# Kernel tuning notes

Hardware: AMD Instinct MI355X
Metric: run time of the kernel (lower is better)

Reference implementation:

```python
import jax, jax.numpy as jnp
import numpy as np

B, SEQ_LEN, PRED_LEN = 256, 96, 96
ENC_IN, LAG = 8, 1
IN_SIZE = ENC_IN + LAG - 1          # 8
H, L = 512, 2
C_OUT = ENC_IN + LAG                # lstm_c_out = 9
TW = SEQ_LEN + PRED_LEN             # train_window = 192


def _mk(key, shape, scale):
    return (jax.random.normal(key, shape, dtype=jnp.float32) * scale)


def setup_inputs() -> dict:
    key = jax.random.key(0)
    ks = jax.random.split(key, 16)
    s_in = 1.0 / np.sqrt(H)
    bih0 = _mk(ks[5], (4 * H,), s_in).at[H:2 * H].set(1.0)  # forget-gate bias init = 1
    bhh0 = _mk(ks[6], (4 * H,), s_in).at[H:2 * H].set(1.0)
    bih1 = _mk(ks[9], (4 * H,), s_in).at[H:2 * H].set(1.0)
    bhh1 = _mk(ks[10], (4 * H,), s_in).at[H:2 * H].set(1.0)
    return {
        "x_enc": jax.random.normal(ks[0], (B, SEQ_LEN, ENC_IN + LAG), dtype=jnp.float32),
        "x_mark_enc": jax.random.normal(ks[1], (B, SEQ_LEN, 4), dtype=jnp.float32),
        "x_dec": jax.random.normal(ks[2], (B, PRED_LEN, ENC_IN + LAG), dtype=jnp.float32),
        "y_enc": jax.random.normal(ks[3], (B, PRED_LEN, ENC_IN + LAG), dtype=jnp.float32),
        "x_mark_dec": jax.random.normal(ks[4], (B, PRED_LEN, 4), dtype=jnp.float32),
        "Wih0": _mk(ks[7], (4 * H, IN_SIZE), s_in),
        "Whh0": _mk(ks[8], (4 * H, H), s_in),
        "bih0": bih0, "bhh0": bhh0,
        "Wih1": _mk(ks[11], (4 * H, H), s_in),
        "Whh1": _mk(ks[12], (4 * H, H), s_in),
        "bih1": bih1, "bhh1": bhh1,
        "Wout": _mk(ks[13], (C_OUT, L * H), 1.0 / np.sqrt(L * H)),
        "bout": _mk(ks[14], (C_OUT,), 1.0 / np.sqrt(L * H)),
    }


def _lstm_cell(x, h, c, Wih, Whh, bih, bhh):
    # gates in torch order: i, f, g, o
    g = x @ Wih.T + bih + h @ Whh.T + bhh           # [B, 4H]
    i, f, gg, o = jnp.split(g, 4, axis=-1)
    c_new = jax.nn.sigmoid(f) * c + jax.nn.sigmoid(i) * jnp.tanh(gg)
    h_new = jax.nn.sigmoid(o) * jnp.tanh(c_new)
    return h_new, c_new


def reference(x_enc, x_mark_enc, x_dec, y_enc, x_mark_dec,
              Wih0, Whh0, bih0, bhh0, Wih1, Whh1, bih1, bhh1, Wout, bout):
    # get_input_data
    batch = jnp.concatenate([x_enc, y_enc[:, -PRED_LEN:, :]], axis=1)  # [B, TW, enc_in+lag]
    train_batch = batch[:, :, :-1]                                     # [B, TW, IN_SIZE]
    xs = jnp.transpose(train_batch, (1, 0, 2))                         # [TW, B, IN_SIZE]

    h0 = jnp.zeros((B, H), jnp.float32)
    init = (h0, h0, h0, h0)  # (h_l0, c_l0, h_l1, c_l1)

    def step(carry, x_t):
        hl0, cl0, hl1, cl1 = carry
        hl0, cl0 = _lstm_cell(x_t, hl0, cl0, Wih0, Whh0, bih0, bhh0)
        hl1, cl1 = _lstm_cell(hl0, hl1, cl1, Wih1, Whh1, bih1, bhh1)
        hidden = jnp.stack([hl0, hl1], axis=0)                 # [L, B, H]
        # get_hidden_permute: permute(1,2,0).view(B, H*L)
        hp = jnp.transpose(hidden, (1, 2, 0)).reshape(B, H * L)
        return (hl0, cl0, hl1, cl1), hp

    _, hps = jax.lax.scan(step, init, xs)                      # [TW, B, H*L]
    hps = jnp.transpose(hps, (1, 0, 2))                        # [B, TW, H*L]
    output_steps = hps @ Wout.T + bout                         # [B, TW, C_OUT]
    return output_steps, batch  # (output_steps, labels_batch); stop_flag always False
```

## Files before the change

kernel.cpp:

```cpp
#include <hip/hip_runtime.h>
#include <hip/hip_cooperative_groups.h>
#include <cstdint>

namespace cg = cooperative_groups;


typedef __bf16 bf16x8 __attribute__((ext_vector_type(8)));
typedef float f32x4 __attribute__((ext_vector_type(4)));

#define SLOT 131072

__device__ __forceinline__ uint16_t f2bf(float f) {
    uint32_t u = __builtin_bit_cast(uint32_t, f);
    u += 0x7FFFu + ((u >> 16) & 1u);
    return (uint16_t)(u >> 16);
}
__device__ __forceinline__ float bf2f(uint16_t h) {
    return __builtin_bit_cast(float, (uint32_t)h << 16);
}
__device__ __forceinline__ float sigm(float x) { return 1.0f / (1.0f + expf(-x)); }

__device__ __forceinline__ bf16x8 ld_h16(const uint16_t* p) {
    const uint64_t* q = (const uint64_t*)p;
    uint64_t w0 = __hip_atomic_load(q,     __ATOMIC_RELAXED, __HIP_MEMORY_SCOPE_AGENT);
    uint64_t w1 = __hip_atomic_load(q + 1, __ATOMIC_RELAXED, __HIP_MEMORY_SCOPE_AGENT);
    union { uint64_t u[2]; bf16x8 v; } x;
    x.u[0] = w0; x.u[1] = w1;
    return x.v;
}
__device__ __forceinline__ uint64_t ld_h64(const uint64_t* q) {
    return __hip_atomic_load(q, __ATOMIC_RELAXED, __HIP_MEMORY_SCOPE_AGENT);
}

__global__ void __launch_bounds__(256, 1)
lstm_kernel(const float* __restrict__ x_enc, const float* __restrict__ y_enc,
            const float* __restrict__ Wih0, const float* __restrict__ Whh0,
            const float* __restrict__ bih0, const float* __restrict__ bhh0,
            const float* __restrict__ Wih1, const float* __restrict__ Whh1,
            const float* __restrict__ bih1, const float* __restrict__ bhh1,
            const float* __restrict__ Wout, const float* __restrict__ bout,
            float* __restrict__ out,
            uint32_t* __restrict__ stamp,
            uint16_t* __restrict__ hs0hi, uint16_t* __restrict__ hs0lo,
            uint16_t* __restrict__ hs1hi, uint16_t* __restrict__ hs1lo)
{
    extern __shared__ __align__(16) uint8_t LDS[];
    float* ldsF = (float*)LDS;

    const int tid = threadIdx.x;
    const int bid = blockIdx.x;
    const bool isL0 = (bid < 128);
    const int rb = isL0 ? bid : (bid - 128);
    const int g = rb >> 6;
    const int s = rb & 63;

    const int w  = tid >> 6;
    const int l  = tid & 63;
    const int c  = l & 15;
    const int kg = l >> 4;
    const int h  = c & 7;
    const bool lowc = (c < 8);

    if (isL0) {
        for (int idx = tid; idx < 32 * 512; idx += 256) {
            int j = idx >> 9, k = idx & 511;
            int n = s * 8 + (j & 7) + 512 * (j >> 3);
            float v = Whh0[n * 512 + k];
            uint16_t hi = f2bf(v);
            uint16_t lo = f2bf(v - bf2f(hi));
            uint32_t byte = (uint32_t)(j * 1024 + k * 2) ^ (uint32_t)((j & 7) << 4);
            *(uint16_t*)(LDS + byte) = hi;
            *(uint16_t*)(LDS + 32768 + byte) = lo;
        }
        {
            int j = tid >> 3, k = tid & 7;
            int n = s * 8 + (j & 7) + 512 * (j >> 3);
            ldsF[17408 + tid] = Wih0[n * 8 + k];
        }
    } else {
        for (int idx = tid; idx < 32 * 1024; idx += 256) {
            int j = idx >> 10, k = idx & 1023;
            int n = s * 8 + (j & 7) + 512 * (j >> 3);
            float v = (k < 512) ? Wih1[n * 512 + k] : Whh1[n * 512 + (k - 512)];
            uint16_t hi = f2bf(v);
            uint16_t lo = f2bf(v - bf2f(hi));
            uint32_t byte = (uint32_t)(j * 2048 + k * 2) ^ (uint32_t)((j & 7) << 4);
            *(uint16_t*)(LDS + byte) = hi;
            *(uint16_t*)(LDS + 65536 + byte) = lo;
        }
    }
    float bias[4];
#pragma unroll
    for (int gt = 0; gt < 4; ++gt) {
        int n = s * 8 + h + 512 * gt;
        bias[gt] = isL0 ? (bih0[n] + bhh0[n]) : (bih1[n] + bhh1[n]);
    }
    {
        int idx = bid * 256 + tid;
        __hip_atomic_store(((uint32_t*)(hs0hi + 3 * SLOT)) + idx, 0u, __ATOMIC_RELAXED, __HIP_MEMORY_SCOPE_AGENT);
        __hip_atomic_store(((uint32_t*)(hs0lo + 3 * SLOT)) + idx, 0u, __ATOMIC_RELAXED, __HIP_MEMORY_SCOPE_AGENT);
        __hip_atomic_store(((uint32_t*)(hs1hi + 3 * SLOT)) + idx, 0u, __ATOMIC_RELAXED, __HIP_MEMORY_SCOPE_AGENT);
        __hip_atomic_store(((uint32_t*)(hs1lo + 3 * SLOT)) + idx, 0u, __ATOMIC_RELAXED, __HIP_MEMORY_SCOPE_AGENT);
    }
    if (tid == 0)
        __hip_atomic_store(&stamp[bid * 16], 0u, __ATOMIC_RELAXED, __HIP_MEMORY_SCOPE_AGENT);
    float creg[4] = {0.f, 0.f, 0.f, 0.f};

    cg::grid_group grid = cg::this_grid();
    grid.sync();

    const int j0 = c, j1 = 16 + c;
    const uint32_t sw0 = (uint32_t)((j0 & 7) << 4);
    const uint32_t sw1 = (uint32_t)((j1 & 7) << 4);

    for (int p = 0; p < 194; ++p) {
        if (p > 0) {
            if (tid < 128) {
                int pid = (tid < 64) ? (g * 64 + tid) : (128 + g * 64 + (tid - 64));
                while (__hip_atomic_load(&stamp[pid * 16], __ATOMIC_RELAXED,
                                         __HIP_MEMORY_SCOPE_AGENT) < (uint32_t)p)
                    __builtin_amdgcn_s_sleep(1);
            }
            __syncthreads();
        }

        if (isL0) {
            const int t = p;
            if (t < 192) {
                for (int idx = tid; idx < 1024; idx += 256) {
                    int bl = idx >> 3, ch = idx & 7;
                    int b = g * 128 + bl;
                    ldsF[16384 + idx] = (t < 96)
                        ? x_enc[(b * 96 + t) * 9 + ch]
                        : y_enc[(b * 96 + (t - 96)) * 9 + ch];
                }
                __syncthreads();

                const uint16_t* hbh = hs0hi + ((t + 3) & 3) * SLOT;
                const uint16_t* hbl = hs0lo + ((t + 3) & 3) * SLOT;
                const int ar0 = (g * 128 + w * 32 + c) * 512 + kg * 8;
                const int ar1 = ar0 + 16 * 512;
                const uint32_t bb0 = (uint32_t)(j0 * 1024 + kg * 16);
                const uint32_t bb1 = (uint32_t)(j1 * 1024 + kg * 16);
                f32x4 acc00 = {0.f,0.f,0.f,0.f}, acc01 = acc00, acc10 = acc00, acc11 = acc00;
#pragma unroll
                for (int ks = 0; ks < 16; ++ks) {
                    bf16x8 a0h = ld_h16(hbh + ar0 + ks * 32);
                    bf16x8 a0l = ld_h16(hbl + ar0 + ks * 32);
                    bf16x8 a1h = ld_h16(hbh + ar1 + ks * 32);
                    bf16x8 a1l = ld_h16(hbl + ar1 + ks * 32);
                    uint32_t o0 = (bb0 + ks * 64) ^ sw0;
                    uint32_t o1 = (bb1 + ks * 64) ^ sw1;
                    bf16x8 b0h = *(const bf16x8*)(LDS + o0);
                    bf16x8 b0l = *(const bf16x8*)(LDS + 32768 + o0);
                    bf16x8 b1h = *(const bf16x8*)(LDS + o1);
                    bf16x8 b1l = *(const bf16x8*)(LDS + 32768 + o1);
                    acc00 = __builtin_amdgcn_mfma_f32_16x16x32_bf16(a0h, b0h, acc00, 0, 0, 0);
                    acc00 = __builtin_amdgcn_mfma_f32_16x16x32_bf16(a0h, b0l, acc00, 0, 0, 0);
                    acc00 = __builtin_amdgcn_mfma_f32_16x16x32_bf16(a0l, b0h, acc00, 0, 0, 0);
                    acc00 = __builtin_amdgcn_mfma_f32_16x16x32_bf16(a0l, b0l, acc00, 0, 0, 0);
                    acc01 = __builtin_amdgcn_mfma_f32_16x16x32_bf16(a0h, b1h, acc01, 0, 0, 0);
                    acc01 = __builtin_amdgcn_mfma_f32_16x16x32_bf16(a0h, b1l, acc01, 0, 0, 0);
                    acc01 = __builtin_amdgcn_mfma_f32_16x16x32_bf16(a0l, b1h, acc01, 0, 0, 0);
                    acc01 = __builtin_amdgcn_mfma_f32_16x16x32_bf16(a0l, b1l, acc01, 0, 0, 0);
                    acc10 = __builtin_amdgcn_mfma_f32_16x16x32_bf16(a1h, b0h, acc10, 0, 0, 0);
                    acc10 = __builtin_amdgcn_mfma_f32_16x16x32_bf16(a1h, b0l, acc10, 0, 0, 0);
                    acc10 = __builtin_amdgcn_mfma_f32_16x16x32_bf16(a1l, b0h, acc10, 0, 0, 0);
                    acc10 = __builtin_amdgcn_mfma_f32_16x16x32_bf16(a1l, b0l, acc10, 0, 0, 0);
                    acc11 = __builtin_amdgcn_mfma_f32_16x16x32_bf16(a1h, b1h, acc11, 0, 0, 0);
                    acc11 = __builtin_amdgcn_mfma_f32_16x16x32_bf16(a1h, b1l, acc11, 0, 0, 0);
                    acc11 = __builtin_amdgcn_mfma_f32_16x16x32_bf16(a1l, b1h, acc11, 0, 0, 0);
                    acc11 = __builtin_amdgcn_mfma_f32_16x16x32_bf16(a1l, b1l, acc11, 0, 0, 0);
                }
                float rv0[4], rv1[4];
#pragma unroll
                for (int r = 0; r < 4; ++r) {
                    rv0[r] = __shfl_xor(lowc ? acc10[r] : acc00[r], 8);
                    rv1[r] = __shfl_xor(lowc ? acc11[r] : acc01[r], 8);
                }
                uint32_t* d32h = (uint32_t*)(hs0hi + (t & 3) * SLOT);
                uint32_t* d32l = (uint32_t*)(hs0lo + (t & 3) * SLOT);
#pragma unroll
                for (int r = 0; r < 4; ++r) {
                    float k0 = lowc ? acc00[r] : acc10[r];
                    float k1 = lowc ? acc01[r] : acc11[r];
                    float gi = lowc ? k0 : rv0[r];
                    float gf = lowc ? rv0[r] : k0;
                    float gG = lowc ? k1 : rv1[r];
                    float go = lowc ? rv1[r] : k1;
                    int m  = (lowc ? 0 : 16) + kg * 4 + r;
                    int bl = w * 32 + m;
                    const float* xr = ldsF + 16384 + bl * 8;
                    const float* wi = ldsF + 17408;
                    float xp0 = 0, xp1 = 0, xp2 = 0, xp3 = 0;
#pragma unroll
                    for (int k = 0; k < 8; ++k) {
                        float xv = xr[k];
                        xp0 += xv * wi[(h) * 8 + k];
                        xp1 += xv * wi[(8 + h) * 8 + k];
                        xp2 += xv * wi[(16 + h) * 8 + k];
                        xp3 += xv * wi[(24 + h) * 8 + k];
                    }
                    gi += xp0 + bias[0];
                    gf += xp1 + bias[1];
                    gG += xp2 + bias[2];
                    go += xp3 + bias[3];
                    float cn = sigm(gf) * creg[r] + sigm(gi) * tanhf(gG);
                    float hn = sigm(go) * tanhf(cn);
                    creg[r] = cn;
                    uint16_t hh = f2bf(hn);
                    uint16_t ll = f2bf(hn - bf2f(hh));
                    uint32_t phi = (uint32_t)__shfl_xor((int)(uint32_t)hh, 1);
                    uint32_t plo = (uint32_t)__shfl_xor((int)(uint32_t)ll, 1);
                    int eoff = ((g * 128 + bl) * 512 + s * 8 + (h & ~1)) >> 1;
                    if ((h & 1) == 0)
                        __hip_atomic_store(d32h + eoff, (uint32_t)hh | (phi << 16),
                                           __ATOMIC_RELAXED, __HIP_MEMORY_SCOPE_AGENT);
                    else
                        __hip_atomic_store(d32l + eoff, plo | ((uint32_t)ll << 16),
                                           __ATOMIC_RELAXED, __HIP_MEMORY_SCOPE_AGENT);
                }
            }
            const int t2 = p - 2;
            if (t2 >= 0) {
                float* ps = ldsF + 17664;
                if (tid < 144) {
                    int bi = tid / 72;
                    int rem = tid % 72;
                    int co = rem >> 3, seg = rem & 7;
                    int b = g * 128 + s * 2 + bi;
                    const uint64_t* p0h = (const uint64_t*)(hs0hi + (t2 & 3) * SLOT + b * 512);
                    const uint64_t* p0l = (const uint64_t*)(hs0lo + (t2 & 3) * SLOT + b * 512);
                    const uint64_t* p1h = (const uint64_t*)(hs1hi + (t2 & 3) * SLOT + b * 512);
                    const uint64_t* p1l = (const uint64_t*)(hs1lo + (t2 & 3) * SLOT + b * 512);
                    const float* wr = Wout + co * 1024;
                    float sum = 0.f;
#pragma unroll 4
                    for (int q = seg * 16; q < seg * 16 + 16; ++q) {
                        uint64_t u0 = ld_h64(p0h + q);
                        uint64_t u1 = ld_h64(p0l + q);
                        uint64_t u2 = ld_h64(p1h + q);
                        uint64_t u3 = ld_h64(p1l + q);
#pragma unroll
                        for (int e = 0; e < 4; ++e) {
                            int hh_ = q * 4 + e;
                            float h0v = bf2f((uint16_t)(u0 >> (16 * e))) + bf2f((uint16_t)(u1 >> (16 * e)));
                            float h1v = bf2f((uint16_t)(u2 >> (16 * e))) + bf2f((uint16_t)(u3 >> (16 * e)));
                            sum += h0v * wr[2 * hh_] + h1v * wr[2 * hh_ + 1];
                        }
                    }
                    ps[tid] = sum;
                }
                __syncthreads();
                if (tid < 18) {
                    int bi = tid / 9, co = tid % 9;
                    float tot = bout[co];
#pragma unroll
                    for (int k2 = 0; k2 < 8; ++k2) tot += ps[bi * 72 + co * 8 + k2];
                    out[((g * 128 + s * 2 + bi) * 192 + t2) * 9 + co] = tot;
                }
            }
        } else {
            const int t = p - 1;
            if (t >= 0 && t < 192) {
                const uint16_t* hbah = hs0hi + (t & 3) * SLOT;
                const uint16_t* hbal = hs0lo + (t & 3) * SLOT;
                const uint16_t* hbbh = hs1hi + ((t + 3) & 3) * SLOT;
                const uint16_t* hbbl = hs1lo + ((t + 3) & 3) * SLOT;
                const int ar0 = (g * 128 + w * 32 + c) * 512 + kg * 8;
                const int ar1 = ar0 + 16 * 512;
                const uint32_t bb0 = (uint32_t)(j0 * 2048 + kg * 16);
                const uint32_t bb1 = (uint32_t)(j1 * 2048 + kg * 16);
                f32x4 acc00 = {0.f,0.f,0.f,0.f}, acc01 = acc00, acc10 = acc00, acc11 = acc00;
#pragma unroll
                for (int ks = 0; ks < 32; ++ks) {
                    const uint16_t* hbh = (ks < 16) ? hbah : hbbh;
                    const uint16_t* hbl = (ks < 16) ? hbal : hbbl;
                    int ko = (ks & 15) * 32;
                    bf16x8 a0h = ld_h16(hbh + ar0 + ko);
                    bf16x8 a0l = ld_h16(hbl + ar0 + ko);
                    bf16x8 a1h = ld_h16(hbh + ar1 + ko);
                    bf16x8 a1l = ld_h16(hbl + ar1 + ko);
                    uint32_t o0 = (bb0 + ks * 64) ^ sw0;
                    uint32_t o1 = (bb1 + ks * 64) ^ sw1;
                    bf16x8 b0h = *(const bf16x8*)(LDS + o0);
                    bf16x8 b0l = *(const bf16x8*)(LDS + 65536 + o0);
                    bf16x8 b1h = *(const bf16x8*)(LDS + o1);
                    bf16x8 b1l = *(const bf16x8*)(LDS + 65536 + o1);
                    acc00 = __builtin_amdgcn_mfma_f32_16x16x32_bf16(a0h, b0h, acc00, 0, 0, 0);
                    acc00 = __builtin_amdgcn_mfma_f32_16x16x32_bf16(a0h, b0l, acc00, 0, 0, 0);
                    acc00 = __builtin_amdgcn_mfma_f32_16x16x32_bf16(a0l, b0h, acc00, 0, 0, 0);
                    acc00 = __builtin_amdgcn_mfma_f32_16x16x32_bf16(a0l, b0l, acc00, 0, 0, 0);
                    acc01 = __builtin_amdgcn_mfma_f32_16x16x32_bf16(a0h, b1h, acc01, 0, 0, 0);
                    acc01 = __builtin_amdgcn_mfma_f32_16x16x32_bf16(a0h, b1l, acc01, 0, 0, 0);
                    acc01 = __builtin_amdgcn_mfma_f32_16x16x32_bf16(a0l, b1h, acc01, 0, 0, 0);
                    acc01 = __builtin_amdgcn_mfma_f32_16x16x32_bf16(a0l, b1l, acc01, 0, 0, 0);
                    acc10 = __builtin_amdgcn_mfma_f32_16x16x32_bf16(a1h, b0h, acc10, 0, 0, 0);
                    acc10 = __builtin_amdgcn_mfma_f32_16x16x32_bf16(a1h, b0l, acc10, 0, 0, 0);
                    acc10 = __builtin_amdgcn_mfma_f32_16x16x32_bf16(a1l, b0h, acc10, 0, 0, 0);
                    acc10 = __builtin_amdgcn_mfma_f32_16x16x32_bf16(a1l, b0l, acc10, 0, 0, 0);
                    acc11 = __builtin_amdgcn_mfma_f32_16x16x32_bf16(a1h, b1h, acc11, 0, 0, 0);
                    acc11 = __builtin_amdgcn_mfma_f32_16x16x32_bf16(a1h, b1l, acc11, 0, 0, 0);
                    acc11 = __builtin_amdgcn_mfma_f32_16x16x32_bf16(a1l, b1h, acc11, 0, 0, 0);
                    acc11 = __builtin_amdgcn_mfma_f32_16x16x32_bf16(a1l, b1l, acc11, 0, 0, 0);
                }
                float rv0[4], rv1[4];
#pragma unroll
                for (int r = 0; r < 4; ++r) {
                    rv0[r] = __shfl_xor(lowc ? acc10[r] : acc00[r], 8);
                    rv1[r] = __shfl_xor(lowc ? acc11[r] : acc01[r], 8);
                }
                uint32_t* d32h = (uint32_t*)(hs1hi + (t & 3) * SLOT);
                uint32_t* d32l = (uint32_t*)(hs1lo + (t & 3) * SLOT);
#pragma unroll
                for (int r = 0; r < 4; ++r) {
                    float k0 = lowc ? acc00[r] : acc10[r];
                    float k1 = lowc ? acc01[r] : acc11[r];
                    float gi = (lowc ? k0 : rv0[r]) + bias[0];
                    float gf = (lowc ? rv0[r] : k0) + bias[1];
                    float gG = (lowc ? k1 : rv1[r]) + bias[2];
                    float go = (lowc ? rv1[r] : k1) + bias[3];
                    int m  = (lowc ? 0 : 16) + kg * 4 + r;
                    int bl = w * 32 + m;
                    float cn = sigm(gf) * creg[r] + sigm(gi) * tanhf(gG);
                    float hn = sigm(go) * tanhf(cn);
                    creg[r] = cn;
                    uint16_t hh = f2bf(hn);
                    uint16_t ll = f2bf(hn - bf2f(hh));
                    uint32_t phi = (uint32_t)__shfl_xor((int)(uint32_t)hh, 1);
                    uint32_t plo = (uint32_t)__shfl_xor((int)(uint32_t)ll, 1);
                    int eoff = ((g * 128 + bl) * 512 + s * 8 + (h & ~1)) >> 1;
                    if ((h & 1) == 0)
                        __hip_atomic_store(d32h + eoff, (uint32_t)hh | (phi << 16),
                                           __ATOMIC_RELAXED, __HIP_MEMORY_SCOPE_AGENT);
                    else
                        __hip_atomic_store(d32l + eoff, plo | ((uint32_t)ll << 16),
                                           __ATOMIC_RELAXED, __HIP_MEMORY_SCOPE_AGENT);
                }
            }
        }

        asm volatile("s_waitcnt vmcnt(0)" ::: "memory");
        __syncthreads();
        if (tid == 0)
            __hip_atomic_store(&stamp[bid * 16], (uint32_t)(p + 1),
                               __ATOMIC_RELAXED, __HIP_MEMORY_SCOPE_AGENT);
    }
}

__global__ void __launch_bounds__(256)
copy_batch(const float* __restrict__ x_enc, const float* __restrict__ y_enc,
           float* __restrict__ out)
{
    int idx = blockIdx.x * 256 + threadIdx.x;
    if (idx >= 256 * 192 * 9) return;
    int b = idx / 1728;
    int rem = idx % 1728;
    int t = rem / 9, ch = rem % 9;
    float v = (t < 96) ? x_enc[b * 864 + t * 9 + ch]
                       : y_enc[b * 864 + (t - 96) * 9 + ch];
    out[442368 + idx] = v;
}

extern "C" void kernel_launch(void* const* d_in, const int* in_sizes, int n_in,
                              void* d_out, int out_size, void* d_ws, size_t ws_size,
                              hipStream_t stream) {
    const float* x_enc = (const float*)d_in[0];
    const float* y_enc = (const float*)d_in[3];
    const float* Wih0  = (const float*)d_in[5];
    const float* Whh0  = (const float*)d_in[6];
    const float* bih0  = (const float*)d_in[7];
    const float* bhh0  = (const float*)d_in[8];
    const float* Wih1  = (const float*)d_in[9];
    const float* Whh1  = (const float*)d_in[10];
    const float* bih1  = (const float*)d_in[11];
    const float* bhh1  = (const float*)d_in[12];
    const float* Wout  = (const float*)d_in[13];
    const float* bout  = (const float*)d_in[14];
    float* out = (float*)d_out;
    uint32_t* stamp = (uint32_t*)d_ws;
    uint16_t* hs0hi = (uint16_t*)((uint8_t*)d_ws + 16384);
    uint16_t* hs0lo = hs0hi + 4 * SLOT;
    uint16_t* hs1hi = hs0lo + 4 * SLOT;
    uint16_t* hs1lo = hs1hi + 4 * SLOT;

    hipLaunchKernelGGL(copy_batch, dim3(1728), dim3(256), 0, stream,
                       x_enc, y_enc, out);

    hipFuncSetAttribute((const void*)lstm_kernel,
                        hipFuncAttributeMaxDynamicSharedMemorySize, 131072);

    void* args[] = { (void*)&x_enc, (void*)&y_enc, (void*)&Wih0, (void*)&Whh0,
                     (void*)&bih0, (void*)&bhh0, (void*)&Wih1, (void*)&Whh1,
                     (void*)&bih1, (void*)&bhh1, (void*)&Wout, (void*)&bout,
                     (void*)&out, (void*)&stamp, (void*)&hs0hi, (void*)&hs0lo,
                     (void*)&hs1hi, (void*)&hs1lo };
    hipLaunchCooperativeKernel((const void*)lstm_kernel, dim3(256), dim3(256),
                               args, 131072, stream);
}
```

Before: 6.198 ms.

## Double waves per block so each wave computes 16 batch rows

Raises the block size from 256 to 512 threads (8 waves), so each wave now owns 16 batch rows instead of 32. That halves the per-wave MFMA chain and the global h loads in each recurrent step. The gate epilogue is remapped so low and high column lanes split the four accumulator rows, and the cell-state registers shrink to two. The intent is to cut per-step latency on the serial recurrence through more wave-level parallelism, at the cost of a tighter per-thread register budget and more threads waiting on each barrier.

```diff
diff --git a/kernel.cpp b/kernel.cpp
--- a/kernel.cpp
+++ b/kernel.cpp
@@ -32,7 +32,7 @@
     return __hip_atomic_load(q, __ATOMIC_RELAXED, __HIP_MEMORY_SCOPE_AGENT);
 }
 
-__global__ void __launch_bounds__(256, 1)
+__global__ void __launch_bounds__(512, 2)
 lstm_kernel(const float* __restrict__ x_enc, const float* __restrict__ y_enc,
             const float* __restrict__ Wih0, const float* __restrict__ Whh0,
             const float* __restrict__ bih0, const float* __restrict__ bhh0,
@@ -62,7 +62,7 @@
     const bool lowc = (c < 8);
 
     if (isL0) {
-        for (int idx = tid; idx < 32 * 512; idx += 256) {
+        for (int idx = tid; idx < 32 * 512; idx += 512) {
             int j = idx >> 9, k = idx & 511;
             int n = s * 8 + (j & 7) + 512 * (j >> 3);
             float v = Whh0[n * 512 + k];
@@ -72,13 +72,13 @@
             *(uint16_t*)(LDS + byte) = hi;
             *(uint16_t*)(LDS + 32768 + byte) = lo;
         }
-        {
+        if (tid < 256) {
             int j = tid >> 3, k = tid & 7;
             int n = s * 8 + (j & 7) + 512 * (j >> 3);
             ldsF[17408 + tid] = Wih0[n * 8 + k];
         }
     } else {
-        for (int idx = tid; idx < 32 * 1024; idx += 256) {
+        for (int idx = tid; idx < 32 * 1024; idx += 512) {
             int j = idx >> 10, k = idx & 1023;
             int n = s * 8 + (j & 7) + 512 * (j >> 3);
             float v = (k < 512) ? Wih1[n * 512 + k] : Whh1[n * 512 + (k - 512)];
@@ -95,7 +95,7 @@
         int n = s * 8 + h + 512 * gt;
         bias[gt] = isL0 ? (bih0[n] + bhh0[n]) : (bih1[n] + bhh1[n]);
     }
-    {
+    if (tid < 256) {
         int idx = bid * 256 + tid;
         __hip_atomic_store(((uint32_t*)(hs0hi + 3 * SLOT)) + idx, 0u, __ATOMIC_RELAXED, __HIP_MEMORY_SCOPE_AGENT);
         __hip_atomic_store(((uint32_t*)(hs0lo + 3 * SLOT)) + idx, 0u, __ATOMIC_RELAXED, __HIP_MEMORY_SCOPE_AGENT);
@@ -104,7 +104,7 @@
     }
     if (tid == 0)
         __hip_atomic_store(&stamp[bid * 16], 0u, __ATOMIC_RELAXED, __HIP_MEMORY_SCOPE_AGENT);
-    float creg[4] = {0.f, 0.f, 0.f, 0.f};
+    float creg[2] = {0.f, 0.f};
 
     cg::grid_group grid = cg::this_grid();
     grid.sync();
@@ -127,7 +127,7 @@
         if (isL0) {
             const int t = p;
             if (t < 192) {
-                for (int idx = tid; idx < 1024; idx += 256) {
+                for (int idx = tid; idx < 1024; idx += 512) {
                     int bl = idx >> 3, ch = idx & 7;
                     int b = g * 128 + bl;
                     ldsF[16384 + idx] = (t < 96)
@@ -138,17 +138,14 @@
 
                 const uint16_t* hbh = hs0hi + ((t + 3) & 3) * SLOT;
                 const uint16_t* hbl = hs0lo + ((t + 3) & 3) * SLOT;
-                const int ar0 = (g * 128 + w * 32 + c) * 512 + kg * 8;
-                const int ar1 = ar0 + 16 * 512;
+                const int ar0 = (g * 128 + w * 16 + c) * 512 + kg * 8;
                 const uint32_t bb0 = (uint32_t)(j0 * 1024 + kg * 16);
                 const uint32_t bb1 = (uint32_t)(j1 * 1024 + kg * 16);
-                f32x4 acc00 = {0.f,0.f,0.f,0.f}, acc01 = acc00, acc10 = acc00, acc11 = acc00;
+                f32x4 acc00 = {0.f,0.f,0.f,0.f}, acc01 = acc00;
 #pragma unroll
                 for (int ks = 0; ks < 16; ++ks) {
                     bf16x8 a0h = ld_h16(hbh + ar0 + ks * 32);
                     bf16x8 a0l = ld_h16(hbl + ar0 + ks * 32);
-                    bf16x8 a1h = ld_h16(hbh + ar1 + ks * 32);
-                    bf16x8 a1l = ld_h16(hbl + ar1 + ks * 32);
                     uint32_t o0 = (bb0 + ks * 64) ^ sw0;
                     uint32_t o1 = (bb1 + ks * 64) ^ sw1;
                     bf16x8 b0h = *(const bf16x8*)(LDS + o0);
@@ -163,33 +160,27 @@
                     acc01 = __builtin_amdgcn_mfma_f32_16x16x32_bf16(a0h, b1l, acc01, 0, 0, 0);
                     acc01 = __builtin_amdgcn_mfma_f32_16x16x32_bf16(a0l, b1h, acc01, 0, 0, 0);
                     acc01 = __builtin_amdgcn_mfma_f32_16x16x32_bf16(a0l, b1l, acc01, 0, 0, 0);
-                    acc10 = __builtin_amdgcn_mfma_f32_16x16x32_bf16(a1h, b0h, acc10, 0, 0, 0);
-                    acc10 = __builtin_amdgcn_mfma_f32_16x16x32_bf16(a1h, b0l, acc10, 0, 0, 0);
-                    acc10 = __builtin_amdgcn_mfma_f32_16x16x32_bf16(a1l, b0h, acc10, 0, 0, 0);
-                    acc10 = __builtin_amdgcn_mfma_f32_16x16x32_bf16(a1l, b0l, acc10, 0, 0, 0);
-                    acc11 = __builtin_amdgcn_mfma_f32_16x16x32_bf16(a1h, b1h, acc11, 0, 0, 0);
-                    acc11 = __builtin_amdgcn_mfma_f32_16x16x32_bf16(a1h, b1l, acc11, 0, 0, 0);
-                    acc11 = __builtin_amdgcn_mfma_f32_16x16x32_bf16(a1l, b1h, acc11, 0, 0, 0);
-                    acc11 = __builtin_amdgcn_mfma_f32_16x16x32_bf16(a1l, b1l, acc11, 0, 0, 0);
                 }
                 float rv0[4], rv1[4];
 #pragma unroll
                 for (int r = 0; r < 4; ++r) {
-                    rv0[r] = __shfl_xor(lowc ? acc10[r] : acc00[r], 8);
-                    rv1[r] = __shfl_xor(lowc ? acc11[r] : acc01[r], 8);
+                    rv0[r] = __shfl_xor(acc00[r], 8);
+                    rv1[r] = __shfl_xor(acc01[r], 8);
                 }
                 uint32_t* d32h = (uint32_t*)(hs0hi + (t & 3) * SLOT);
                 uint32_t* d32l = (uint32_t*)(hs0lo + (t & 3) * SLOT);
 #pragma unroll
-                for (int r = 0; r < 4; ++r) {
-                    float k0 = lowc ? acc00[r] : acc10[r];
-                    float k1 = lowc ? acc01[r] : acc11[r];
-                    float gi = lowc ? k0 : rv0[r];
-                    float gf = lowc ? rv0[r] : k0;
-                    float gG = lowc ? k1 : rv1[r];
-                    float go = lowc ? rv1[r] : k1;
-                    int m  = (lowc ? 0 : 16) + kg * 4 + r;
-                    int bl = w * 32 + m;
+                for (int rr = 0; rr < 2; ++rr) {
+                    const float k0   = lowc ? acc00[rr] : acc00[rr + 2];
+                    const float k1   = lowc ? acc01[rr] : acc01[rr + 2];
+                    const float rv0v = lowc ? rv0[rr]   : rv0[rr + 2];
+                    const float rv1v = lowc ? rv1[rr]   : rv1[rr + 2];
+                    float gi = lowc ? k0 : rv0v;
+                    float gf = lowc ? rv0v : k0;
+                    float gG = lowc ? k1 : rv1v;
+                    float go = lowc ? rv1v : k1;
+                    const int r = (lowc ? 0 : 2) + rr;
+                    int bl = w * 16 + kg * 4 + r;
                     const float* xr = ldsF + 16384 + bl * 8;
                     const float* wi = ldsF + 17408;
                     float xp0 = 0, xp1 = 0, xp2 = 0, xp3 = 0;
@@ -205,9 +196,9 @@
                     gf += xp1 + bias[1];
                     gG += xp2 + bias[2];
                     go += xp3 + bias[3];
-                    float cn = sigm(gf) * creg[r] + sigm(gi) * tanhf(gG);
+                    float cn = sigm(gf) * creg[rr] + sigm(gi) * tanhf(gG);
                     float hn = sigm(go) * tanhf(cn);
-                    creg[r] = cn;
+                    creg[rr] = cn;
                     uint16_t hh = f2bf(hn);
                     uint16_t ll = f2bf(hn - bf2f(hh));
                     uint32_t phi = (uint32_t)__shfl_xor((int)(uint32_t)hh, 1);
@@ -267,11 +258,10 @@
                 const uint16_t* hbal = hs0lo + (t & 3) * SLOT;
                 const uint16_t* hbbh = hs1hi + ((t + 3) & 3) * SLOT;
                 const uint16_t* hbbl = hs1lo + ((t + 3) & 3) * SLOT;
-                const int ar0 = (g * 128 + w * 32 + c) * 512 + kg * 8;
-                const int ar1 = ar0 + 16 * 512;
+                const int ar0 = (g * 128 + w * 16 + c) * 512 + kg * 8;
                 const uint32_t bb0 = (uint32_t)(j0 * 2048 + kg * 16);
                 const uint32_t bb1 = (uint32_t)(j1 * 2048 + kg * 16);
-                f32x4 acc00 = {0.f,0.f,0.f,0.f}, acc01 = acc00, acc10 = acc00, acc11 = acc00;
+                f32x4 acc00 = {0.f,0.f,0.f,0.f}, acc01 = acc00;
 #pragma unroll
                 for (int ks = 0; ks < 32; ++ks) {
                     const uint16_t* hbh = (ks < 16) ? hbah : hbbh;
@@ -279,8 +269,6 @@
                     int ko = (ks & 15) * 32;
                     bf16x8 a0h = ld_h16(hbh + ar0 + ko);
                     bf16x8 a0l = ld_h16(hbl + ar0 + ko);
-                    bf16x8 a1h = ld_h16(hbh + ar1 + ko);
-                    bf16x8 a1l = ld_h16(hbl + ar1 + ko);
                     uint32_t o0 = (bb0 + ks * 64) ^ sw0;
                     uint32_t o1 = (bb1 + ks * 64) ^ sw1;
                     bf16x8 b0h = *(const bf16x8*)(LDS + o0);
@@ -295,36 +283,30 @@
                     acc01 = __builtin_amdgcn_mfma_f32_16x16x32_bf16(a0h, b1l, acc01, 0, 0, 0);
                     acc01 = __builtin_amdgcn_mfma_f32_16x16x32_bf16(a0l, b1h, acc01, 0, 0, 0);
                     acc01 = __builtin_amdgcn_mfma_f32_16x16x32_bf16(a0l, b1l, acc01, 0, 0, 0);
-                    acc10 = __builtin_amdgcn_mfma_f32_16x16x32_bf16(a1h, b0h, acc10, 0, 0, 0);
-                    acc10 = __builtin_amdgcn_mfma_f32_16x16x32_bf16(a1h, b0l, acc10, 0, 0, 0);
-                    acc10 = __builtin_amdgcn_mfma_f32_16x16x32_bf16(a1l, b0h, acc10, 0, 0, 0);
-                    acc10 = __builtin_amdgcn_mfma_f32_16x16x32_bf16(a1l, b0l, acc10, 0, 0, 0);
-                    acc11 = __builtin_amdgcn_mfma_f32_16x16x32_bf16(a1h, b1h, acc11, 0, 0, 0);
-                    acc11 = __builtin_amdgcn_mfma_f32_16x16x32_bf16(a1h, b1l, acc11, 0, 0, 0);
-                    acc11 = __builtin_amdgcn_mfma_f32_16x16x32_bf16(a1l, b1h, acc11, 0, 0, 0);
-                    acc11 = __builtin_amdgcn_mfma_f32_16x16x32_bf16(a1l, b1l, acc11, 0, 0, 0);
                 }
                 float rv0[4], rv1[4];
 #pragma unroll
                 for (int r = 0; r < 4; ++r) {
-                    rv0[r] = __shfl_xor(lowc ? acc10[r] : acc00[r], 8);
-                    rv1[r] = __shfl_xor(lowc ? acc11[r] : acc01[r], 8);
+                    rv0[r] = __shfl_xor(acc00[r], 8);
+                    rv1[r] = __shfl_xor(acc01[r], 8);
                 }
                 uint32_t* d32h = (uint32_t*)(hs1hi + (t & 3) * SLOT);
                 uint32_t* d32l = (uint32_t*)(hs1lo + (t & 3) * SLOT);
 #pragma unroll
-                for (int r = 0; r < 4; ++r) {
-                    float k0 = lowc ? acc00[r] : acc10[r];
-                    float k1 = lowc ? acc01[r] : acc11[r];
-                    float gi = (lowc ? k0 : rv0[r]) + bias[0];
-                    float gf = (lowc ? rv0[r] : k0) + bias[1];
-                    float gG = (lowc ? k1 : rv1[r]) + bias[2];
-                    float go = (lowc ? rv1[r] : k1) + bias[3];
-                    int m  = (lowc ? 0 : 16) + kg * 4 + r;
-                    int bl = w * 32 + m;
-                    float cn = sigm(gf) * creg[r] + sigm(gi) * tanhf(gG);
+                for (int rr = 0; rr < 2; ++rr) {
+                    const float k0   = lowc ? acc00[rr] : acc00[rr + 2];
+                    const float k1   = lowc ? acc01[rr] : acc01[rr + 2];
+                    const float rv0v = lowc ? rv0[rr]   : rv0[rr + 2];
+                    const float rv1v = lowc ? rv1[rr]   : rv1[rr + 2];
+                    float gi = (lowc ? k0 : rv0v) + bias[0];
+                    float gf = (lowc ? rv0v : k0) + bias[1];
+                    float gG = (lowc ? k1 : rv1v) + bias[2];
+                    float go = (lowc ? rv1v : k1) + bias[3];
+                    const int r = (lowc ? 0 : 2) + rr;
+                    int bl = w * 16 + kg * 4 + r;
+                    float cn = sigm(gf) * creg[rr] + sigm(gi) * tanhf(gG);
                     float hn = sigm(go) * tanhf(cn);
-                    creg[r] = cn;
+                    creg[rr] = cn;
                     uint16_t hh = f2bf(hn);
                     uint16_t ll = f2bf(hn - bf2f(hh));
                     uint32_t phi = (uint32_t)__shfl_xor((int)(uint32_t)hh, 1);
@@ -395,6 +377,6 @@
                      (void*)&bih1, (void*)&bhh1, (void*)&Wout, (void*)&bout,
                      (void*)&out, (void*)&stamp, (void*)&hs0hi, (void*)&hs0lo,
                      (void*)&hs1hi, (void*)&hs1lo };
-    hipLaunchCooperativeKernel((const void*)lstm_kernel, dim3(256), dim3(256),
+    hipLaunchCooperativeKernel((const void*)lstm_kernel, dim3(256), dim3(512),
                                args, 131072, stream);
 }
```

Result: no change. 6.158 ms (-0.6%).
